# Performance work log

Hardware: AMD Instinct MI355X
Metric: run time of the kernel (lower is better)

Reference implementation:

```python
import jax, jax.numpy as jnp
import numpy as np

N = 50000   # nodes
E = 400000  # edges (before self-loops)
F = 128     # num_features
H = 8       # heads (layer 1)
C = 64      # hidden_channels
B = 64      # graphs in batch
K = 10      # num_classes
NEG_SLOPE = 0.2


def setup_inputs() -> dict:
    key = jax.random.key(0)
    ks = jax.random.split(key, 12)
    g = lambda k, shape, fan: jax.random.normal(k, shape, jnp.float32) / np.sqrt(fan).astype(np.float32)
    return {
        "x": jax.random.normal(ks[0], (N, F), jnp.float32),
        "edge_index": jax.random.randint(ks[1], (2, E), 0, N, jnp.int32),
        "batch": jnp.sort(jax.random.randint(ks[2], (N,), 0, B, jnp.int32)),
        "W1": g(ks[3], (F, H * C), F),
        "att_src1": g(ks[4], (H, C), C),
        "att_dst1": g(ks[5], (H, C), C),
        "b1": jnp.zeros((H * C,), jnp.float32),
        "W2": g(ks[6], (H * C, C), H * C),
        "att_src2": g(ks[7], (1, C), C),
        "att_dst2": g(ks[8], (1, C), C),
        "b2": jnp.zeros((C,), jnp.float32),
        "lin1_w": g(ks[9], (C, C), C),
        "lin1_b": jnp.zeros((C,), jnp.float32),
        "lin2_w": g(ks[10], (C, K), C),
        "lin2_b": jnp.zeros((K,), jnp.float32),
    }


def gat_conv(x, src, dst, W, att_src, att_dst, bias):
    """PyG GATConv (self-loops already appended to src/dst). x:[N,Fin] -> [N,H*C]."""
    heads, out_c = att_src.shape
    h = (x @ W).reshape(N, heads, out_c)                      # [N,H,C]
    a_s = jnp.einsum('nhc,hc->nh', h, att_src)                # [N,H]
    a_d = jnp.einsum('nhc,hc->nh', h, att_dst)
    e = jax.nn.leaky_relu(a_s[src] + a_d[dst], NEG_SLOPE)     # [E',H]
    # segment softmax over incoming edges of each destination node
    m = jax.ops.segment_max(e, dst, num_segments=N)
    e = jnp.exp(e - m[dst])
    denom = jax.ops.segment_sum(e, dst, num_segments=N)
    alpha = e / (denom[dst] + 1e-16)                          # [E',H]
    out = jax.ops.segment_sum(h[src] * alpha[:, :, None], dst, num_segments=N)  # [N,H,C]
    return out.reshape(N, heads * out_c) + bias


def reference(x, edge_index, batch, W1, att_src1, att_dst1, b1,
              W2, att_src2, att_dst2, b2, lin1_w, lin1_b, lin2_w, lin2_b):
    loops = jnp.arange(N, dtype=edge_index.dtype)
    src = jnp.concatenate([edge_index[0], loops])
    dst = jnp.concatenate([edge_index[1], loops])

    h = gat_conv(x, src, dst, W1, att_src1, att_dst1, b1)     # [N, H*C]
    h = jax.nn.elu(h)                                         # dropout inactive (eval)
    h = gat_conv(h, src, dst, W2, att_src2, att_dst2, b2)     # [N, C]
    h = jax.nn.elu(h)

    pooled = jax.ops.segment_sum(h, batch, num_segments=B)    # global_add_pool -> [B, C]
    z = jax.nn.elu(pooled @ lin1_w + lin1_b)
    logits = z @ lin2_w + lin2_b
    return jax.nn.log_softmax(logits, axis=-1)
```

## Files before the change

kernel.cpp:

```cpp
#include <hip/hip_runtime.h>
#include <hip/hip_bf16.h>

#define DEV static __device__ __forceinline__

constexpr int F1 = 128;
constexpr int H1 = 8;
constexpr int C  = 64;
constexpr int B  = 64;
constexpr int K  = 10;
constexpr float NEG = 0.2f;

typedef __attribute__((ext_vector_type(8))) short short8;
typedef __attribute__((ext_vector_type(4))) float floatx4;
typedef __attribute__((ext_vector_type(2))) float floatx2;

DEV float b2f(__hip_bfloat16 x) { return __bfloat162float(x); }
DEV float elu1(float v) { return v > 0.f ? v : (__expf(v) - 1.f); }
DEV unsigned short f2bbits(float f) {
  __hip_bfloat16 b = __float2bfloat16(f);
  return *(unsigned short*)&b;
}
DEV float blo(unsigned u) { return __uint_as_float(u << 16); }
DEV float bhi(unsigned u) { return __uint_as_float(u & 0xffff0000u); }
DEV float bu(unsigned short u) { return __uint_as_float(((unsigned)u) << 16); }
DEV unsigned pack2(float lo, float hi) {
  return (unsigned)f2bbits(lo) | ((unsigned)f2bbits(hi) << 16);
}
DEV float rcp_nr(float x) {
  float r = __builtin_amdgcn_rcpf(x);
  return r * (2.f - x * r);
}
DEV void pk_fma(floatx2& acc, floatx2 x, floatx2 w) {
  asm("v_pk_fma_f32 %0, %1, %2, %0" : "+v"(acc) : "v"(x), "s"(w));
}
DEV void pk_add(floatx2& acc, floatx2 w) {
  asm("v_pk_add_f32 %0, %0, %1" : "+v"(acc) : "s"(w));
}


DEV int detect_dev(const void* xraw, int* lds) {
  if (threadIdx.x == 0) {
    const __hip_bfloat16* xb = (const __hip_bfloat16*)xraw;
    int bad = 0;
    for (int i = 0; i < 128; ++i) {
      float v = b2f(xb[2 * i]);
      if (!(fabsf(v) < 1e4f)) bad++;
    }
    *lds = (bad < 13) ? 1 : 0;
  }
  __syncthreads();
  return *lds;
}

#define CVT(p, i) (isbf ? b2f(((const __hip_bfloat16*)(p))[i]) : ((const float*)(p))[i])

__global__ void fused_prep_kernel(const void* x_raw, const void* w1raw,
                                  const void* as1r, const void* ad1r, const void* b1r,
                                  const void* w2raw,
                                  const void* as2r, const void* ad2r, const void* b2r,
                                  const void* l1wr, const void* l1br,
                                  const void* l2wr, const void* l2br,
                                  unsigned short* __restrict__ xbf,
                                  unsigned short* __restrict__ w1frag,
                                  unsigned short* __restrict__ w2frag,
                                  unsigned short* __restrict__ vfrag,
                                  float* __restrict__ wts,
                                  int* __restrict__ deg,
                                  float* __restrict__ pooled,
                                  int nX, int N) {
  __shared__ int fl;
  int isbf = detect_dev(x_raw, &fl);
  int gid = blockIdx.x * 256 + threadIdx.x;
  int stride = gridDim.x * 256;

  if (isbf) {
    const unsigned short* src = (const unsigned short*)x_raw;
    for (int i = gid; i < nX; i += stride) xbf[i] = src[i];
  } else {
    const float* src = (const float*)x_raw;
    for (int i = gid; i < nX; i += stride) xbf[i] = f2bbits(src[i]);
  }
  for (int i = gid; i < 512;  i += stride) {
    int hp = i >> 7, l16 = (i >> 3) & 15, nt = i & 7;
    int c = hp * 128 + nt * 16 + l16;
    wts[1024 + i] = CVT(b1r, c);
  }
  for (int i = gid; i < 64;   i += stride) wts[1536 + i] = CVT(as2r, i);
  for (int i = gid; i < 64;   i += stride) wts[1600 + i] = CVT(ad2r, i);
  for (int i = gid; i < 64;   i += stride) wts[1664 + i] = CVT(b2r, i);
  for (int i = gid; i < 4096; i += stride) wts[1728 + i] = CVT(l1wr, i);
  for (int i = gid; i < 64;   i += stride) wts[5824 + i] = CVT(l1br, i);
  for (int i = gid; i < 640;  i += stride) wts[5888 + i] = CVT(l2wr, i);
  for (int i = gid; i < 10;   i += stride) wts[6528 + i] = CVT(l2br, i);
  for (int t = gid; t < 8192; t += stride) {
    int lane = t & 63, ks = (t >> 6) & 3, nt = t >> 8;
    for (int j = 0; j < 8; ++j) {
      int k = ks * 32 + (lane >> 4) * 8 + j;
      int n = nt * 16 + (lane & 15);
      w1frag[t * 8 + j] = f2bbits(CVT(w1raw, k * 512 + n));
    }
  }
  for (int t = gid; t < 4096; t += stride) {
    int lane = t & 63, nt = (t >> 6) & 3, ks = t >> 8;
    for (int j = 0; j < 8; ++j) {
      int p = ks * 32 + (lane >> 4) * 8 + j;
      int hp = p >> 7, pl16 = (p >> 3) & 15, pnt = p & 7;
      int k = hp * 128 + pnt * 16 + pl16;
      int n = nt * 16 + (lane & 15);
      w2frag[t * 8 + j] = f2bbits(CVT(w2raw, k * 64 + n));
    }
  }
  for (int t = gid; t < 2048; t += stride) {
    int j = t & 7, lane = (t >> 3) & 63, ks = t >> 9;
    int k = ks * 32 + (lane >> 4) * 8 + j;
    int n = lane & 15;
    int hh = (n < 8) ? n : (n - 8);
    float s = 0.f;
    if (n < 8) {
      for (int c = 0; c < 64; ++c)
        s += CVT(w1raw, k * 512 + hh * 64 + c) * CVT(as1r, hh * 64 + c);
    } else {
      for (int c = 0; c < 64; ++c)
        s += CVT(w1raw, k * 512 + hh * 64 + c) * CVT(ad1r, hh * 64 + c);
    }
    vfrag[(ks * 64 + lane) * 8 + j] = f2bbits(s);
  }
  for (int i = gid; i < N; i += stride) deg[i] = 0;
  for (int i = gid; i < B * C; i += stride) pooled[i] = 0.f;
}

__global__ void deg_count_kernel(const int* __restrict__ ei, int E, int Etot,
                                 int* __restrict__ deg) {
  int e = blockIdx.x * blockDim.x + threadIdx.x;
  if (e >= Etot) return;
  int d = (e < E) ? ei[E + e] : e - E;
  atomicAdd(&deg[d], 1);
}

__global__ void scan_block_kernel(const int* __restrict__ deg,
                                  int* __restrict__ local,
                                  int* __restrict__ bsum, int N) {
  __shared__ int tmp[256];
  int t = threadIdx.x;
  int i = blockIdx.x * 256 + t;
  int v = (i < N) ? deg[i] : 0;
  tmp[t] = v;
  __syncthreads();
  for (int off = 1; off < 256; off <<= 1) {
    int u = (t >= off) ? tmp[t - off] : 0;
    __syncthreads();
    tmp[t] += u;
    __syncthreads();
  }
  if (i < N) local[i] = tmp[t] - v;
  if (t == 255) bsum[blockIdx.x] = tmp[255];
}

__global__ void scan_finish_kernel(const int* __restrict__ local,
                                   const int* __restrict__ bsum, int nb,
                                   int* __restrict__ rowptr,
                                   int* __restrict__ cursor, int N, int Etot) {
  __shared__ int tmp[256];
  __shared__ int offs;
  int t = threadIdx.x;
  int v0 = (t < nb) ? bsum[t] : 0;
  tmp[t] = v0;
  __syncthreads();
  for (int off = 1; off < 256; off <<= 1) {
    int u = (t >= off) ? tmp[t - off] : 0;
    __syncthreads();
    tmp[t] += u;
    __syncthreads();
  }
  if (t == (int)blockIdx.x) offs = tmp[t] - v0;
  __syncthreads();
  int i = blockIdx.x * 256 + t;
  if (i < N) {
    int r = local[i] + offs;
    rowptr[i] = r;
    cursor[i] = r;
  }
  if (i == 0) rowptr[N] = Etot;
}

__global__ __launch_bounds__(256) void att_scalars_kernel(
    const unsigned short* __restrict__ xbf,
    const unsigned short* __restrict__ vfrag,
    float* __restrict__ a_s, float* __restrict__ a_d,
    int N) {
  int t = threadIdx.x, w = t >> 6, lane = t & 63;
  int quad = lane >> 4, l16 = lane & 15;
  int row0 = blockIdx.x * 64 + w * 16;

  floatx4 acc = {};
  int rl = row0 + l16; if (rl >= N) rl = N - 1;
  const unsigned short* xp = xbf + (size_t)rl * 128 + quad * 8;
#pragma unroll
  for (int ks = 0; ks < 4; ++ks) {
    short8 a = *(const short8*)(xp + ks * 32);
    short8 b = *(const short8*)&vfrag[(ks * 64 + lane) * 8];
    acc = __builtin_amdgcn_mfma_f32_16x16x32_bf16(a, b, acc, 0, 0, 0);
  }
#pragma unroll
  for (int r = 0; r < 4; ++r) {
    int row = row0 + quad * 4 + r;
    if (row < N) {
      if (l16 < 8) a_s[(size_t)row * 8 + l16] = acc[r];
      else         a_d[(size_t)row * 8 + (l16 - 8)] = acc[r];
    }
  }
}

__global__ void fill_weight_kernel(const int* __restrict__ ei, int E, int Etot,
                                   const float* __restrict__ a_s,
                                   const float* __restrict__ a_d,
                                   int* __restrict__ cursor,
                                   int* __restrict__ col,
                                   float* __restrict__ wedge) {
  int e = blockIdx.x * 256 + threadIdx.x;
  if (e >= Etot) return;
  int s, d;
  if (e < E) { s = ei[e]; d = ei[E + e]; } else { s = d = e - E; }
  int pos = atomicAdd(&cursor[d], 1);
  col[pos] = s;
  float4 s0 = *(const float4*)(a_s + (size_t)s * 8);
  float4 s1 = *(const float4*)(a_s + (size_t)s * 8 + 4);
  float4 d0 = *(const float4*)(a_d + (size_t)d * 8);
  float4 d1 = *(const float4*)(a_d + (size_t)d * 8 + 4);
  float4 w0, w1;
  float v;
  v = s0.x + d0.x; v = v > 0.f ? v : NEG * v; w0.x = __expf(v);
  v = s0.y + d0.y; v = v > 0.f ? v : NEG * v; w0.y = __expf(v);
  v = s0.z + d0.z; v = v > 0.f ? v : NEG * v; w0.z = __expf(v);
  v = s0.w + d0.w; v = v > 0.f ? v : NEG * v; w0.w = __expf(v);
  v = s1.x + d1.x; v = v > 0.f ? v : NEG * v; w1.x = __expf(v);
  v = s1.y + d1.y; v = v > 0.f ? v : NEG * v; w1.y = __expf(v);
  v = s1.z + d1.z; v = v > 0.f ? v : NEG * v; w1.z = __expf(v);
  v = s1.w + d1.w; v = v > 0.f ? v : NEG * v; w1.w = __expf(v);
  *(float4*)(wedge + (size_t)pos * 8)     = w0;
  *(float4*)(wedge + (size_t)pos * 8 + 4) = w1;
}

__global__ __launch_bounds__(512, 8) void aggx_gemm1_kernel(
    const unsigned short* __restrict__ xbf,
    const unsigned short* __restrict__ W1frag,
    const int* __restrict__ rowptr,
    const int* __restrict__ col,
    const float* __restrict__ wedge,
    const float* __restrict__ bias_perm,
    unsigned short* __restrict__ out1,
    int N) {
  __shared__ __align__(16) unsigned short Agg[8 * 8 * 144];
  int t = threadIdx.x, w = t >> 6, lane = t & 63;
  int dbase = blockIdx.x * 8;
  const unsigned* xd = (const unsigned*)xbf;
  unsigned* AggU = (unsigned*)Agg;

  {
    int d = dbase + w;
    int dd = d < N ? d : N - 1;
    int beg = rowptr[dd], end = rowptr[dd + 1];
    floatx2 acc[8] = {};
    floatx2 dn01 = {}, dn23 = {}, dn45 = {}, dn67 = {};
#pragma unroll 2
    for (int i = beg; i < end; ++i) {
      int iu = __builtin_amdgcn_readfirstlane(i);
      int s = col[iu];
      unsigned xv = xd[((size_t)s << 6) + lane];
      const float* wp = wedge + (size_t)iu * 8;
      float w0 = wp[0], w1 = wp[1], w2 = wp[2], w3 = wp[3];
      float w4 = wp[4], w5 = wp[5], w6 = wp[6], w7 = wp[7];
      floatx2 p01 = {w0, w1}, p23 = {w2, w3}, p45 = {w4, w5}, p67 = {w6, w7};
      pk_add(dn01, p01); pk_add(dn23, p23);
      pk_add(dn45, p45); pk_add(dn67, p67);
      floatx2 xp; xp.x = blo(xv); xp.y = bhi(xv);
      floatx2 b0 = {w0, w0}, b1 = {w1, w1}, b2 = {w2, w2}, b3 = {w3, w3};
      floatx2 b4 = {w4, w4}, b5 = {w5, w5}, b6 = {w6, w6}, b7 = {w7, w7};
      pk_fma(acc[0], xp, b0); pk_fma(acc[1], xp, b1);
      pk_fma(acc[2], xp, b2); pk_fma(acc[3], xp, b3);
      pk_fma(acc[4], xp, b4); pk_fma(acc[5], xp, b5);
      pk_fma(acc[6], xp, b6); pk_fma(acc[7], xp, b7);
    }
    float inv[8];
    inv[0] = rcp_nr(dn01.x + 1e-16f); inv[1] = rcp_nr(dn01.y + 1e-16f);
    inv[2] = rcp_nr(dn23.x + 1e-16f); inv[3] = rcp_nr(dn23.y + 1e-16f);
    inv[4] = rcp_nr(dn45.x + 1e-16f); inv[5] = rcp_nr(dn45.y + 1e-16f);
    inv[6] = rcp_nr(dn67.x + 1e-16f); inv[7] = rcp_nr(dn67.y + 1e-16f);
#pragma unroll
    for (int h = 0; h < 8; ++h)
      AggU[(h * 8 + w) * 72 + lane] =
          pack2(acc[h].x * inv[h], acc[h].y * inv[h]);
  }
  __syncthreads();

  {
    int quad = lane >> 4, l16 = lane & 15;
    int hp = w >> 1, q = w & 1;
    int h = hp * 2 + q;
    floatx4 acc2[4] = {};
    const unsigned short* Bp = W1frag + (size_t)hp * 16384;
#pragma unroll
    for (int ks = 0; ks < 4; ++ks) {
      short8 a = *(const short8*)&Agg[(h * 8 + (l16 & 7)) * 144 + ks * 32 + quad * 8];
#pragma unroll
      for (int j = 0; j < 4; ++j) {
        int nt = q * 4 + j;
        short8 b = *(const short8*)&Bp[((nt * 4 + ks) * 64 + lane) * 8];
        acc2[j] = __builtin_amdgcn_mfma_f32_16x16x32_bf16(a, b, acc2[j], 0, 0, 0);
      }
    }
    float4 bq = *(const float4*)&bias_perm[hp * 128 + l16 * 8 + q * 4];
#pragma unroll
    for (int r = 0; r < 4; ++r) {
      int dl = quad * 4 + r;
      int row = dbase + dl;
      if (dl < 8 && row < N) {
        uint2 o;
        o.x = pack2(elu1(acc2[0][r] + bq.x), elu1(acc2[1][r] + bq.y));
        o.y = pack2(elu1(acc2[2][r] + bq.z), elu1(acc2[3][r] + bq.w));
        *(uint2*)&out1[(size_t)row * 512 + hp * 128 + l16 * 8 + q * 4] = o;
      }
    }
  }
}

__global__ __launch_bounds__(256) void gemm2_mfma_kernel(
    const unsigned short* __restrict__ x2bf,
    const unsigned short* __restrict__ W2frag,
    const float* __restrict__ att_src,
    const float* __restrict__ att_dst,
    unsigned short* __restrict__ h2,
    float* __restrict__ a_s, float* __restrict__ a_d,
    int N) {
  int t = threadIdx.x;
  int w = t >> 6, lane = t & 63;
  int quad = lane >> 4, l16 = lane & 15;
  int rowbase = blockIdx.x * 64 + w * 16;

  floatx4 acc[4] = {};
  int r0 = rowbase + l16; if (r0 >= N) r0 = N - 1;
  const unsigned short* p0 = x2bf + (size_t)r0 * 512 + quad * 8;
#pragma unroll
  for (int ks = 0; ks < 16; ++ks) {
    short8 a0 = *(const short8*)(p0 + ks * 32);
#pragma unroll
    for (int nt = 0; nt < 4; ++nt) {
      short8 b = *(const short8*)&W2frag[((ks * 4 + nt) * 64 + lane) * 8];
      acc[nt] = __builtin_amdgcn_mfma_f32_16x16x32_bf16(a0, b, acc[nt], 0, 0, 0);
    }
  }

  float asw[4], adw[4];
#pragma unroll
  for (int nt = 0; nt < 4; ++nt) {
    asw[nt] = att_src[nt * 16 + l16];
    adw[nt] = att_dst[nt * 16 + l16];
  }
  float ps[4] = {}, pd[4] = {};
#pragma unroll
  for (int nt = 0; nt < 4; ++nt)
#pragma unroll
    for (int r = 0; r < 4; ++r) {
      float v = acc[nt][r];
      int row = rowbase + quad * 4 + r;
      if (row < N) h2[(size_t)row * 64 + nt * 16 + l16] = f2bbits(v);
      ps[r] += v * asw[nt];
      pd[r] += v * adw[nt];
    }
#pragma unroll
  for (int r = 0; r < 4; ++r) {
    float p = ps[r], q = pd[r];
#pragma unroll
    for (int off = 1; off < 16; off <<= 1) {
      p += __shfl_xor(p, off);
      q += __shfl_xor(q, off);
    }
    int row = rowbase + quad * 4 + r;
    if (l16 == 0 && row < N) {
      a_s[row] = p;
      a_d[row] = q;
    }
  }
}

__global__ void gat_agg1_kernel(const int* __restrict__ rowptr,
                                const int* __restrict__ col,
                                const float* __restrict__ a_s,
                                const float* __restrict__ a_d,
                                const unsigned short* __restrict__ hfeat,
                                const float* __restrict__ bias,
                                unsigned short* __restrict__ out, int N) {
  int wave = threadIdx.x >> 6, lane = threadIdx.x & 63;
  int d = blockIdx.x * 4 + wave;
  if (d >= N) return;
  int beg = rowptr[d], end = rowptr[d + 1];
  int qg = lane >> 4, l16 = lane & 15;
  float adv = a_d[d];
  const uint2* hfu = (const uint2*)hfeat;
  float acc[4] = {};
  float wsum = 0.f;
#pragma unroll 2
  for (int i = beg + qg; i < end; i += 4) {
    int s = col[i];
    float v = a_s[s] + adv;
    v = v > 0.f ? v : NEG * v;
    float wv = __expf(v);
    wsum += wv;
    uint2 u = hfu[(size_t)s * 16 + l16];
    acc[0] += wv * blo(u.x); acc[1] += wv * bhi(u.x);
    acc[2] += wv * blo(u.y); acc[3] += wv * bhi(u.y);
  }
#pragma unroll
  for (int off = 16; off <= 32; off <<= 1) {
#pragma unroll
    for (int j = 0; j < 4; ++j) acc[j] += __shfl_xor(acc[j], off);
    wsum += __shfl_xor(wsum, off);
  }
  float winv = 1.f / (wsum + 1e-16f);
  float4 bb = ((const float4*)bias)[l16];
  float r0 = elu1(acc[0] * winv + bb.x), r1 = elu1(acc[1] * winv + bb.y);
  float r2 = elu1(acc[2] * winv + bb.z), r3 = elu1(acc[3] * winv + bb.w);
  if (qg == 0) {
    uint2 o; o.x = pack2(r0, r1); o.y = pack2(r2, r3);
    ((uint2*)out)[(size_t)d * 16 + l16] = o;
  }
}

__global__ void pool_kernel(const unsigned short* __restrict__ out2,
                            const int* __restrict__ batch,
                            float* __restrict__ pooled, int N) {
  int wave = threadIdx.x >> 6, lane = threadIdx.x & 63;
  int seg = blockIdx.x * 4 + wave;
  int start = seg * 16;
  if (start >= N) return;
  int end = min(start + 16, N);
  int cur = batch[start];
  float acc = 0.f;
  for (int n = start; n < end; ++n) {
    int bn = batch[n];
    if (bn != cur) {
      unsafeAtomicAdd(&pooled[cur * 64 + lane], acc);
      acc = 0.f; cur = bn;
    }
    acc += bu(out2[(size_t)n * 64 + lane]);
  }
  unsafeAtomicAdd(&pooled[cur * 64 + lane], acc);
}

__global__ void head_kernel(const float* __restrict__ pooled,
                            const float* __restrict__ lin1_w,
                            const float* __restrict__ lin1_b,
                            const float* __restrict__ lin2_w,
                            const float* __restrict__ lin2_b,
                            const void* __restrict__ x_raw,
                            void* __restrict__ outv) {
  __shared__ float P[C];
  __shared__ float Zs[C];
  __shared__ float Ls[K];
  __shared__ float lse_s;
  __shared__ int fl;
  int isbf = detect_dev(x_raw, &fl);
  int g = blockIdx.x, t = threadIdx.x;
  P[t] = pooled[g * C + t];
  __syncthreads();
  float acc = lin1_b[t];
  for (int k = 0; k < C; ++k) acc += P[k] * lin1_w[k * C + t];
  Zs[t] = elu1(acc);
  __syncthreads();
  if (t < K) {
    float a = lin2_b[t];
    for (int k = 0; k < C; ++k) a += Zs[k] * lin2_w[k * K + t];
    Ls[t] = a;
  }
  __syncthreads();
  if (t == 0) {
    float mx = -1e30f;
    for (int c = 0; c < K; ++c) mx = fmaxf(mx, Ls[c]);
    float s = 0.f;
    for (int c = 0; c < K; ++c) s += __expf(Ls[c] - mx);
    lse_s = mx + __logf(s);
  }
  __syncthreads();
  if (t < K) {
    float val = Ls[t] - lse_s;
    if (isbf) ((__hip_bfloat16*)outv)[g * K + t] = __float2bfloat16(val);
    else      ((float*)outv)[g * K + t] = val;
  }
}

extern "C" void kernel_launch(void* const* d_in, const int* in_sizes, int n_in,
                              void* d_out, int out_size, void* d_ws, size_t ws_size,
                              hipStream_t stream) {
  const void* x_raw = d_in[0];
  const int*  ei    = (const int*)d_in[1];
  const int*  batch = (const int*)d_in[2];

  const int N    = in_sizes[2];
  const int E    = in_sizes[1] / 2;
  const int Etot = E + N;
  const int nb   = (N + 255) / 256;

  float* ws   = (float*)d_ws;
  size_t off  = 0;

  float* wts = ws + off; off += 6544;
  float* b1w  = wts + 1024;
  float* as2w = wts + 1536;
  float* ad2w = wts + 1600;
  float* b2w  = wts + 1664;
  float* l1w  = wts + 1728;
  float* l1b  = wts + 5824;
  float* l2w  = wts + 5888;
  float* l2b  = wts + 6528;

  unsigned short* xbf    = (unsigned short*)(ws + off); off += (size_t)N * 64;
  unsigned short* w1frag = (unsigned short*)(ws + off); off += 32768;
  unsigned short* w2frag = (unsigned short*)(ws + off); off += 16384;
  unsigned short* vfrag  = (unsigned short*)(ws + off); off += 1024;
  float* wedge           = ws + off;                    off += (size_t)Etot * 8;
  unsigned short* out1bf = (unsigned short*)(ws + off); off += (size_t)N * 256;
  unsigned short* h2bf   = (unsigned short*)(ws + off); off += (size_t)N * 32;
  unsigned short* out2bf = (unsigned short*)(ws + off); off += (size_t)N * 32;
  float* as1  = ws + off; off += (size_t)N * H1;
  float* ad1  = ws + off; off += (size_t)N * H1;
  float* as2  = ws + off; off += (size_t)N;
  float* ad2  = ws + off; off += (size_t)N;
  float* pooled = ws + off; off += (size_t)B * C;

  int* ibase  = (int*)(ws + off);
  int* deg    = ibase;                 ibase += N;
  int* cursor = ibase;                 ibase += N;
  int* rowptr = ibase;                 ibase += N + 1;
  int* locals = ibase;                 ibase += N;
  int* bsum   = ibase;                 ibase += 256;
  int* col    = ibase;                 ibase += Etot;

  fused_prep_kernel<<<1024, 256, 0, stream>>>(
      x_raw, d_in[3], d_in[4], d_in[5], d_in[6], d_in[7], d_in[8], d_in[9],
      d_in[10], d_in[11], d_in[12], d_in[13], d_in[14],
      xbf, w1frag, w2frag, vfrag, wts, deg, pooled, in_sizes[0], N);

  deg_count_kernel<<<(Etot + 255) / 256, 256, 0, stream>>>(ei, E, Etot, deg);
  scan_block_kernel<<<nb, 256, 0, stream>>>(deg, locals, bsum, N);
  scan_finish_kernel<<<nb, 256, 0, stream>>>(locals, bsum, nb, rowptr, cursor, N, Etot);

  att_scalars_kernel<<<(N + 63) / 64, 256, 0, stream>>>(xbf, vfrag, as1, ad1, N);

  fill_weight_kernel<<<(Etot + 255) / 256, 256, 0, stream>>>(
      ei, E, Etot, as1, ad1, cursor, col, wedge);

  aggx_gemm1_kernel<<<(N + 7) / 8, 512, 0, stream>>>(
      xbf, w1frag, rowptr, col, wedge, b1w, out1bf, N);

  gemm2_mfma_kernel<<<(N + 63) / 64, 256, 0, stream>>>(out1bf, w2frag, as2w, ad2w,
                                                       h2bf, as2, ad2, N);
  gat_agg1_kernel<<<(N + 3) / 4, 256, 0, stream>>>(rowptr, col, as2, ad2, h2bf, b2w, out2bf, N);

  pool_kernel<<<(N + 63) / 64, 256, 0, stream>>>(out2bf, batch, pooled, N);
  head_kernel<<<B, 64, 0, stream>>>(pooled, l1w, l1b, l2w, l2b, x_raw, (void*)d_out);
}
```

Baseline: 303.8 us.

## Balance layer-1 aggregation by splitting block edges evenly across waves

```diff
diff --git a/kernel.cpp b/kernel.cpp
--- a/kernel.cpp
+++ b/kernel.cpp
@@ -95,7 +95,8 @@
   for (int t = gid; t < 8192; t += stride) {
     int lane = t & 63, ks = (t >> 6) & 3, nt = t >> 8;
     for (int j = 0; j < 8; ++j) {
-      int k = ks * 32 + (lane >> 4) * 8 + j;
+      int kp = ks * 32 + (lane >> 4) * 8 + j;
+      int k = (kp < 64) ? (2 * kp) : (2 * (kp - 64) + 1);
       int n = nt * 16 + (lane & 15);
       w1frag[t * 8 + j] = f2bbits(CVT(w1raw, k * 512 + n));
     }
@@ -250,63 +251,116 @@
     const float* __restrict__ bias_perm,
     unsigned short* __restrict__ out1,
     int N) {
-  __shared__ __align__(16) unsigned short Agg[8 * 8 * 144];
-  int t = threadIdx.x, w = t >> 6, lane = t & 63;
+  __shared__ float AggF[8 * 8 * 132];
+  __shared__ float DN[64];
+  int t = threadIdx.x;
+  int w = __builtin_amdgcn_readfirstlane(t >> 6);
+  int lane = t & 63;
   int dbase = blockIdx.x * 8;
   const unsigned* xd = (const unsigned*)xbf;
-  unsigned* AggU = (unsigned*)Agg;
+
+  for (int k = t; k < 8 * 8 * 132; k += 512) AggF[k] = 0.f;
+  if (t < 64) DN[t] = 0.f;
+  __syncthreads();
 
   {
-    int d = dbase + w;
-    int dd = d < N ? d : N - 1;
-    int beg = rowptr[dd], end = rowptr[dd + 1];
-    floatx2 acc[8] = {};
-    floatx2 dn01 = {}, dn23 = {}, dn45 = {}, dn67 = {};
-#pragma unroll 2
-    for (int i = beg; i < end; ++i) {
-      int iu = __builtin_amdgcn_readfirstlane(i);
-      int s = col[iu];
-      unsigned xv = xd[((size_t)s << 6) + lane];
-      const float* wp = wedge + (size_t)iu * 8;
-      float w0 = wp[0], w1 = wp[1], w2 = wp[2], w3 = wp[3];
-      float w4 = wp[4], w5 = wp[5], w6 = wp[6], w7 = wp[7];
-      floatx2 p01 = {w0, w1}, p23 = {w2, w3}, p45 = {w4, w5}, p67 = {w6, w7};
-      pk_add(dn01, p01); pk_add(dn23, p23);
-      pk_add(dn45, p45); pk_add(dn67, p67);
-      floatx2 xp; xp.x = blo(xv); xp.y = bhi(xv);
-      floatx2 b0 = {w0, w0}, b1 = {w1, w1}, b2 = {w2, w2}, b3 = {w3, w3};
-      floatx2 b4 = {w4, w4}, b5 = {w5, w5}, b6 = {w6, w6}, b7 = {w7, w7};
-      pk_fma(acc[0], xp, b0); pk_fma(acc[1], xp, b1);
-      pk_fma(acc[2], xp, b2); pk_fma(acc[3], xp, b3);
-      pk_fma(acc[4], xp, b4); pk_fma(acc[5], xp, b5);
-      pk_fma(acc[6], xp, b6); pk_fma(acc[7], xp, b7);
-    }
-    float inv[8];
-    inv[0] = rcp_nr(dn01.x + 1e-16f); inv[1] = rcp_nr(dn01.y + 1e-16f);
-    inv[2] = rcp_nr(dn23.x + 1e-16f); inv[3] = rcp_nr(dn23.y + 1e-16f);
-    inv[4] = rcp_nr(dn45.x + 1e-16f); inv[5] = rcp_nr(dn45.y + 1e-16f);
-    inv[6] = rcp_nr(dn67.x + 1e-16f); inv[7] = rcp_nr(dn67.y + 1e-16f);
-#pragma unroll
-    for (int h = 0; h < 8; ++h)
-      AggU[(h * 8 + w) * 72 + lane] =
-          pack2(acc[h].x * inv[h], acc[h].y * inv[h]);
+    int R0 = rowptr[dbase];
+    int R8 = rowptr[min(dbase + 8, N)];
+    int L  = R8 - R0;
+    int CH = (L + 7) >> 3;
+    int ib = R0 + w * CH;
+    int ie = min(ib + CH, R8);
+    if (ib < ie) {
+      int d = 0;
+      while (d < 7 && rowptr[min(dbase + d + 1, N)] <= ib) ++d;
+      int nxt = rowptr[min(dbase + d + 1, N)];
+      floatx2 a0 = {}, a1 = {}, a2 = {}, a3 = {};
+      floatx2 a4 = {}, a5 = {}, a6 = {}, a7 = {};
+      floatx2 dn01 = {}, dn23 = {}, dn45 = {}, dn67 = {};
+      bool touched = false;
+      auto flush = [&](int dc) {
+        atomicAdd(&AggF[(0 * 8 + dc) * 132 + lane], a0.x);
+        atomicAdd(&AggF[(0 * 8 + dc) * 132 + 64 + lane], a0.y);
+        atomicAdd(&AggF[(1 * 8 + dc) * 132 + lane], a1.x);
+        atomicAdd(&AggF[(1 * 8 + dc) * 132 + 64 + lane], a1.y);
+        atomicAdd(&AggF[(2 * 8 + dc) * 132 + lane], a2.x);
+        atomicAdd(&AggF[(2 * 8 + dc) * 132 + 64 + lane], a2.y);
+        atomicAdd(&AggF[(3 * 8 + dc) * 132 + lane], a3.x);
+        atomicAdd(&AggF[(3 * 8 + dc) * 132 + 64 + lane], a3.y);
+        atomicAdd(&AggF[(4 * 8 + dc) * 132 + lane], a4.x);
+        atomicAdd(&AggF[(4 * 8 + dc) * 132 + 64 + lane], a4.y);
+        atomicAdd(&AggF[(5 * 8 + dc) * 132 + lane], a5.x);
+        atomicAdd(&AggF[(5 * 8 + dc) * 132 + 64 + lane], a5.y);
+        atomicAdd(&AggF[(6 * 8 + dc) * 132 + lane], a6.x);
+        atomicAdd(&AggF[(6 * 8 + dc) * 132 + 64 + lane], a6.y);
+        atomicAdd(&AggF[(7 * 8 + dc) * 132 + lane], a7.x);
+        atomicAdd(&AggF[(7 * 8 + dc) * 132 + 64 + lane], a7.y);
+        if (lane == 0) {
+          atomicAdd(&DN[0 * 8 + dc], dn01.x);
+          atomicAdd(&DN[1 * 8 + dc], dn01.y);
+          atomicAdd(&DN[2 * 8 + dc], dn23.x);
+          atomicAdd(&DN[3 * 8 + dc], dn23.y);
+          atomicAdd(&DN[4 * 8 + dc], dn45.x);
+          atomicAdd(&DN[5 * 8 + dc], dn45.y);
+          atomicAdd(&DN[6 * 8 + dc], dn67.x);
+          atomicAdd(&DN[7 * 8 + dc], dn67.y);
+        }
+      };
+      auto zero = [&]() {
+        a0 = a1 = a2 = a3 = a4 = a5 = a6 = a7 = (floatx2){0.f, 0.f};
+        dn01 = dn23 = dn45 = dn67 = (floatx2){0.f, 0.f};
+      };
+      for (int i = ib; i < ie; ++i) {
+        while (i >= nxt) {
+          if (touched) { flush(d); zero(); touched = false; }
+          ++d;
+          nxt = rowptr[min(dbase + d + 1, N)];
+        }
+        int s = __builtin_amdgcn_readfirstlane(col[i]);
+        const float* wp = wedge + (size_t)i * 8;
+        float w0 = wp[0], w1 = wp[1], w2 = wp[2], w3 = wp[3];
+        float w4 = wp[4], w5 = wp[5], w6 = wp[6], w7 = wp[7];
+        floatx2 p01 = {w0, w1}, p23 = {w2, w3}, p45 = {w4, w5}, p67 = {w6, w7};
+        pk_add(dn01, p01); pk_add(dn23, p23);
+        pk_add(dn45, p45); pk_add(dn67, p67);
+        unsigned xv = xd[((size_t)s << 6) + lane];
+        floatx2 xp; xp.x = blo(xv); xp.y = bhi(xv);
+        floatx2 b0 = {w0, w0}, b1 = {w1, w1}, b2 = {w2, w2}, b3 = {w3, w3};
+        floatx2 b4 = {w4, w4}, b5 = {w5, w5}, b6 = {w6, w6}, b7 = {w7, w7};
+        pk_fma(a0, xp, b0); pk_fma(a1, xp, b1);
+        pk_fma(a2, xp, b2); pk_fma(a3, xp, b3);
+        pk_fma(a4, xp, b4); pk_fma(a5, xp, b5);
+        pk_fma(a6, xp, b6); pk_fma(a7, xp, b7);
+        touched = true;
+      }
+      if (touched) flush(d);
+    }
   }
   __syncthreads();
 
   {
     int quad = lane >> 4, l16 = lane & 15;
     int hp = w >> 1, q = w & 1;
-    int h = hp * 2 + q;
+    int h = w;
+    int d8 = l16 & 7;
+    float invd = rcp_nr(DN[h * 8 + d8] + 1e-16f);
     floatx4 acc2[4] = {};
     const unsigned short* Bp = W1frag + (size_t)hp * 16384;
 #pragma unroll
     for (int ks = 0; ks < 4; ++ks) {
-      short8 a = *(const short8*)&Agg[(h * 8 + (l16 & 7)) * 144 + ks * 32 + quad * 8];
+      const float* ap = &AggF[(h * 8 + d8) * 132 + ks * 32 + quad * 8];
+      float4 f0 = *(const float4*)ap;
+      float4 f1 = *(const float4*)(ap + 4);
+      union { short8 s; unsigned u[4]; } cv;
+      cv.u[0] = pack2(f0.x * invd, f0.y * invd);
+      cv.u[1] = pack2(f0.z * invd, f0.w * invd);
+      cv.u[2] = pack2(f1.x * invd, f1.y * invd);
+      cv.u[3] = pack2(f1.z * invd, f1.w * invd);
 #pragma unroll
       for (int j = 0; j < 4; ++j) {
         int nt = q * 4 + j;
         short8 b = *(const short8*)&Bp[((nt * 4 + ks) * 64 + lane) * 8];
-        acc2[j] = __builtin_amdgcn_mfma_f32_16x16x32_bf16(a, b, acc2[j], 0, 0, 0);
+        acc2[j] = __builtin_amdgcn_mfma_f32_16x16x32_bf16(cv.s, b, acc2[j], 0, 0, 0);
       }
     }
     float4 bq = *(const float4*)&bias_perm[hp * 128 + l16 * 8 + q * 4];
```

After: 725.4 us. +138.8%, slower.

## Recast layer-1 weighted neighbor aggregation as MFMA over 32-edge chunks

Applied to the files above, without the earlier changes.

```diff
diff --git a/kernel.cpp b/kernel.cpp
--- a/kernel.cpp
+++ b/kernel.cpp
@@ -12,7 +12,6 @@
 
 typedef __attribute__((ext_vector_type(8))) short short8;
 typedef __attribute__((ext_vector_type(4))) float floatx4;
-typedef __attribute__((ext_vector_type(2))) float floatx2;
 
 DEV float b2f(__hip_bfloat16 x) { return __bfloat162float(x); }
 DEV float elu1(float v) { return v > 0.f ? v : (__expf(v) - 1.f); }
@@ -29,12 +28,6 @@
 DEV float rcp_nr(float x) {
   float r = __builtin_amdgcn_rcpf(x);
   return r * (2.f - x * r);
-}
-DEV void pk_fma(floatx2& acc, floatx2 x, floatx2 w) {
-  asm("v_pk_fma_f32 %0, %1, %2, %0" : "+v"(acc) : "v"(x), "s"(w));
-}
-DEV void pk_add(floatx2& acc, floatx2 w) {
-  asm("v_pk_add_f32 %0, %0, %1" : "+v"(acc) : "s"(w));
 }
 
 
@@ -241,7 +234,7 @@
   *(float4*)(wedge + (size_t)pos * 8 + 4) = w1;
 }
 
-__global__ __launch_bounds__(512, 8) void aggx_gemm1_kernel(
+__global__ __launch_bounds__(512, 4) void aggx_gemm1_kernel(
     const unsigned short* __restrict__ xbf,
     const unsigned short* __restrict__ W1frag,
     const int* __restrict__ rowptr,
@@ -250,75 +243,125 @@
     const float* __restrict__ bias_perm,
     unsigned short* __restrict__ out1,
     int N) {
-  __shared__ __align__(16) unsigned short Agg[8 * 8 * 144];
+  __shared__ __align__(16) unsigned short XgT[128 * 32];
+  __shared__ __align__(16) unsigned short Wm[8 * 16 * 32];
+  __shared__ __align__(16) unsigned short AggP[8 * 16 * 136];
+  __shared__ int rpl[17];
+
   int t = threadIdx.x, w = t >> 6, lane = t & 63;
-  int dbase = blockIdx.x * 8;
-  const unsigned* xd = (const unsigned*)xbf;
-  unsigned* AggU = (unsigned*)Agg;
+  int q = lane >> 4, n = lane & 15;
+  int dbase = blockIdx.x * 16;
+
+  if (t < 17) rpl[t] = rowptr[min(dbase + t, N)];
+  __syncthreads();
+  int R0 = rpl[0], R1 = rpl[16];
+  int nch = (R1 - R0 + 31) >> 5;
+
+  int ke = t >> 4, p = t & 15;
+  int dw = t >> 5, kw = t & 31;
+
+  short8 onesf = {};
+  if (n == 0) {
+#pragma unroll
+    for (int j = 0; j < 8; ++j) onesf[j] = (short)0x3F80;
+  }
+
+  floatx4 accw[8] = {};
+  floatx4 accdn = {};
+
+  for (int c = 0; c < nch; ++c) {
+    int ebase = R0 + c * 32;
+    __syncthreads();
+
+    {
+      int e = ebase + ke;
+      int ec = (e < R1) ? e : (R1 - 1);
+      int s = col[ec];
+      uint4 xv = *(const uint4*)(xbf + (size_t)s * 128 + p * 8);
+      int xb = (512 * p + 2 * ke) ^ ((p & 3) << 4);
+      unsigned short* xp0 = (unsigned short*)((char*)XgT + xb);
+      xp0[0]   = (unsigned short)(xv.x & 0xffff);
+      xp0[32]  = (unsigned short)(xv.x >> 16);
+      xp0[64]  = (unsigned short)(xv.y & 0xffff);
+      xp0[96]  = (unsigned short)(xv.y >> 16);
+      xp0[128] = (unsigned short)(xv.z & 0xffff);
+      xp0[160] = (unsigned short)(xv.z >> 16);
+      xp0[192] = (unsigned short)(xv.w & 0xffff);
+      xp0[224] = (unsigned short)(xv.w >> 16);
+    }
+    {
+      int ew = ebase + kw;
+      bool evw = ew < R1;
+      int ewc = evw ? ew : (R1 - 1);
+      int dl = 0;
+#pragma unroll
+      for (int b = 8; b; b >>= 1) dl += (rpl[dl + b] <= ew) ? b : 0;
+      float4 wa = *(const float4*)(wedge + (size_t)ewc * 8);
+      float4 wb = *(const float4*)(wedge + (size_t)ewc * 8 + 4);
+      bool mine = evw && (dl == dw);
+      unsigned short z = 0;
+      unsigned short* wmp = Wm + dw * 32 + kw;
+      wmp[0]    = mine ? f2bbits(wa.x) : z;
+      wmp[512]  = mine ? f2bbits(wa.y) : z;
+      wmp[1024] = mine ? f2bbits(wa.z) : z;
+      wmp[1536] = mine ? f2bbits(wa.w) : z;
+      wmp[2048] = mine ? f2bbits(wb.x) : z;
+      wmp[2560] = mine ? f2bbits(wb.y) : z;
+      wmp[3072] = mine ? f2bbits(wb.z) : z;
+      wmp[3584] = mine ? f2bbits(wb.w) : z;
+    }
+    __syncthreads();
+
+    short8 af = *(const short8*)(Wm + w * 512 + n * 32 + 8 * q);
+    accdn = __builtin_amdgcn_mfma_f32_16x16x32_bf16(af, onesf, accdn, 0, 0, 0);
+#pragma unroll
+    for (int ft = 0; ft < 8; ++ft) {
+      int bb = (ft * 16 + n) * 64 + 16 * q;
+      bb ^= ((bb >> 9) & 3) << 4;
+      short8 bfr = *(const short8*)((const char*)XgT + bb);
+      accw[ft] = __builtin_amdgcn_mfma_f32_16x16x32_bf16(af, bfr, accw[ft], 0, 0, 0);
+    }
+  }
 
   {
-    int d = dbase + w;
-    int dd = d < N ? d : N - 1;
-    int beg = rowptr[dd], end = rowptr[dd + 1];
-    floatx2 acc[8] = {};
-    floatx2 dn01 = {}, dn23 = {}, dn45 = {}, dn67 = {};
-#pragma unroll 2
-    for (int i = beg; i < end; ++i) {
-      int iu = __builtin_amdgcn_readfirstlane(i);
-      int s = col[iu];
-      unsigned xv = xd[((size_t)s << 6) + lane];
-      const float* wp = wedge + (size_t)iu * 8;
-      float w0 = wp[0], w1 = wp[1], w2 = wp[2], w3 = wp[3];
-      float w4 = wp[4], w5 = wp[5], w6 = wp[6], w7 = wp[7];
-      floatx2 p01 = {w0, w1}, p23 = {w2, w3}, p45 = {w4, w5}, p67 = {w6, w7};
-      pk_add(dn01, p01); pk_add(dn23, p23);
-      pk_add(dn45, p45); pk_add(dn67, p67);
-      floatx2 xp; xp.x = blo(xv); xp.y = bhi(xv);
-      floatx2 b0 = {w0, w0}, b1 = {w1, w1}, b2 = {w2, w2}, b3 = {w3, w3};
-      floatx2 b4 = {w4, w4}, b5 = {w5, w5}, b6 = {w6, w6}, b7 = {w7, w7};
-      pk_fma(acc[0], xp, b0); pk_fma(acc[1], xp, b1);
-      pk_fma(acc[2], xp, b2); pk_fma(acc[3], xp, b3);
-      pk_fma(acc[4], xp, b4); pk_fma(acc[5], xp, b5);
-      pk_fma(acc[6], xp, b6); pk_fma(acc[7], xp, b7);
-    }
-    float inv[8];
-    inv[0] = rcp_nr(dn01.x + 1e-16f); inv[1] = rcp_nr(dn01.y + 1e-16f);
-    inv[2] = rcp_nr(dn23.x + 1e-16f); inv[3] = rcp_nr(dn23.y + 1e-16f);
-    inv[4] = rcp_nr(dn45.x + 1e-16f); inv[5] = rcp_nr(dn45.y + 1e-16f);
-    inv[6] = rcp_nr(dn67.x + 1e-16f); inv[7] = rcp_nr(dn67.y + 1e-16f);
-#pragma unroll
-    for (int h = 0; h < 8; ++h)
-      AggU[(h * 8 + w) * 72 + lane] =
-          pack2(acc[h].x * inv[h], acc[h].y * inv[h]);
+    float dnv[4];
+#pragma unroll
+    for (int r = 0; r < 4; ++r) {
+      float dr = __shfl(accdn[r], lane & 48);
+      dnv[r] = rcp_nr(dr + 1e-16f);
+    }
+#pragma unroll
+    for (int ft = 0; ft < 8; ++ft)
+#pragma unroll
+      for (int r = 0; r < 4; ++r)
+        AggP[w * 2176 + (4 * q + r) * 136 + ft * 16 + n] =
+            f2bbits(accw[ft][r] * dnv[r]);
   }
   __syncthreads();
 
   {
-    int quad = lane >> 4, l16 = lane & 15;
-    int hp = w >> 1, q = w & 1;
-    int h = hp * 2 + q;
+    int hp = w >> 1, qq = w & 1;
     floatx4 acc2[4] = {};
     const unsigned short* Bp = W1frag + (size_t)hp * 16384;
 #pragma unroll
     for (int ks = 0; ks < 4; ++ks) {
-      short8 a = *(const short8*)&Agg[(h * 8 + (l16 & 7)) * 144 + ks * 32 + quad * 8];
+      short8 a2 = *(const short8*)&AggP[w * 2176 + n * 136 + ks * 32 + q * 8];
 #pragma unroll
       for (int j = 0; j < 4; ++j) {
-        int nt = q * 4 + j;
-        short8 b = *(const short8*)&Bp[((nt * 4 + ks) * 64 + lane) * 8];
-        acc2[j] = __builtin_amdgcn_mfma_f32_16x16x32_bf16(a, b, acc2[j], 0, 0, 0);
+        int nt = qq * 4 + j;
+        short8 b2 = *(const short8*)&Bp[((nt * 4 + ks) * 64 + lane) * 8];
+        acc2[j] = __builtin_amdgcn_mfma_f32_16x16x32_bf16(a2, b2, acc2[j], 0, 0, 0);
       }
     }
-    float4 bq = *(const float4*)&bias_perm[hp * 128 + l16 * 8 + q * 4];
+    float4 bq = *(const float4*)&bias_perm[hp * 128 + n * 8 + qq * 4];
 #pragma unroll
     for (int r = 0; r < 4; ++r) {
-      int dl = quad * 4 + r;
-      int row = dbase + dl;
-      if (dl < 8 && row < N) {
+      int row = dbase + 4 * q + r;
+      if (row < N) {
         uint2 o;
         o.x = pack2(elu1(acc2[0][r] + bq.x), elu1(acc2[1][r] + bq.y));
         o.y = pack2(elu1(acc2[2][r] + bq.z), elu1(acc2[3][r] + bq.w));
-        *(uint2*)&out1[(size_t)row * 512 + hp * 128 + l16 * 8 + q * 4] = o;
+        *(uint2*)&out1[(size_t)row * 512 + hp * 128 + n * 8 + qq * 4] = o;
       }
     }
   }
@@ -549,7 +592,7 @@
   fill_weight_kernel<<<(Etot + 255) / 256, 256, 0, stream>>>(
       ei, E, Etot, as1, ad1, cursor, col, wedge);
 
-  aggx_gemm1_kernel<<<(N + 7) / 8, 512, 0, stream>>>(
+  aggx_gemm1_kernel<<<(N + 15) / 16, 512, 0, stream>>>(
       xbf, w1frag, rowptr, col, wedge, b1w, out1bf, N);
 
   gemm2_mfma_kernel<<<(N + 63) / 64, 256, 0, stream>>>(out1bf, w2frag, as2w, ad2w,
```

Result: faster. 296.5 us (-2.4%).
